# Optimization experiments

Hardware: AMD Instinct MI355X
Metric: run time of the kernel (lower is better)

Reference implementation:

```python
import jax, jax.numpy as jnp
import numpy as np

B, I, H = 128, 512, 512


def setup_inputs() -> dict:
    key = jax.random.key(0)
    ks = jax.random.split(key, 6)
    std = float(1.0 / np.sqrt(H))
    return {
        "x": jax.random.normal(ks[0], (B, I), jnp.float32),
        "h_prev": jax.random.normal(ks[1], (B, H), jnp.float32),
        "C_prev": jax.random.normal(ks[2], (B, H, H), jnp.float32),
        "m_prev": jnp.zeros((B, H), jnp.float32),
        "n_prev": jax.random.normal(ks[3], (B, H), jnp.float32),
        "W": jax.random.uniform(ks[4], (6 * H, I), jnp.float32, -std, std),
        "b": jax.random.uniform(ks[5], (6 * H,), jnp.float32, -std, std),
    }


def reference(x, h_prev, C_prev, m_prev, n_prev, W, b):
    # gates: [B, 6H] -> six [B, H] slices (input, forget, output, query, key, value)
    gates = x @ W.T + b
    ig, fg, og, q, k, v = jnp.split(gates, 6, axis=1)
    inv_sqrt_h = jnp.float32(1.0 / np.sqrt(H))
    k_t = inv_sqrt_h * k
    o_t = jax.nn.sigmoid(og)
    # log-domain stabilizer: log(exp(fg)) == fg, log(exp(ig)) == ig
    m_t = jnp.maximum(fg + m_prev, ig)
    i_t = jnp.exp(ig - m_t)
    f_t = jnp.exp(fg + m_prev - m_t)
    # matrix state update: broadcast-add of (i*v*k) column across last dim (as in source)
    C_t = f_t[:, :, None] * C_prev + (i_t * v * k_t)[:, :, None]  # [B,H,H]
    n_t = f_t * n_prev + i_t * k_t  # [B,H]
    # read-out: C_t @ q and n_t . q
    Cq = jnp.einsum("bij,bj->bi", C_t, q)  # [B,H]
    nq = jnp.einsum("bh,bh->b", n_t, q)  # [B]
    denom = jnp.maximum(jnp.abs(nq), jnp.float32(1e-6))
    h_t = o_t * (Cq / denom[:, None])
    return h_t, C_t, m_t, n_t
```

## Files before the change

### kernel.cpp

```cpp
#include <hip/hip_runtime.h>
#include <math.h>


#define B_SZ   128
#define H_DIM  512
#define I_DIM  512
#define G6     3072
#define BH     65536
#define CSZ    33554432

__global__ __launch_bounds__(256) void gemm_gates(
    const float* __restrict__ x, const float* __restrict__ W,
    const float* __restrict__ bias, float* __restrict__ gates) {
  const int tid = threadIdx.x;
  const int c   = (blockIdx.x % 12) * 256 + tid;
  const int b0  = (blockIdx.x / 12) * 8;

  float acc[8];
#pragma unroll
  for (int j = 0; j < 8; ++j) acc[j] = 0.0f;

  const float4* wrow = reinterpret_cast<const float4*>(W + (size_t)c * I_DIM);
  const float4* x4   = reinterpret_cast<const float4*>(x);

  for (int t4 = 0; t4 < I_DIM / 4; ++t4) {
    float4 wv = wrow[t4];
#pragma unroll
    for (int j = 0; j < 8; ++j) {
      float4 xv = x4[(b0 + j) * (I_DIM / 4) + t4];
      acc[j] += xv.x * wv.x + xv.y * wv.y + xv.z * wv.z + xv.w * wv.w;
    }
  }
  const float bi = bias[c];
#pragma unroll
  for (int j = 0; j < 8; ++j)
    gates[(size_t)(b0 + j) * G6 + c] = acc[j] + bi;
}

__global__ __launch_bounds__(256) void gate_pointwise(
    const float* __restrict__ gates, const float* __restrict__ m_prev,
    const float* __restrict__ n_prev, float* __restrict__ out,
    float* __restrict__ f_arr, float* __restrict__ add_arr,
    float* __restrict__ o_arr, float* __restrict__ invden) {
  const int b   = blockIdx.x;
  const int tid = threadIdx.x;
  const float inv_sqrt_h = 0.044194173824159216f;

  const float* g = gates + (size_t)b * G6;
  float* out_m = out + BH + CSZ;
  float* out_n = out_m + BH;

  float local = 0.0f;
  for (int h = tid; h < H_DIM; h += 256) {
    const float ig = g[h];
    const float fg = g[512 + h];
    const float og = g[1024 + h];
    const float q  = g[1536 + h];
    const float k  = g[2048 + h];
    const float v  = g[2560 + h];

    const int   idx = b * H_DIM + h;
    const float kt  = inv_sqrt_h * k;
    const float ot  = 1.0f / (1.0f + expf(-og));
    const float mp  = m_prev[idx];
    const float npv = n_prev[idx];
    const float mt  = fmaxf(fg + mp, ig);
    const float it  = expf(ig - mt);
    const float ft  = expf(fg + mp - mt);
    const float nt  = ft * npv + it * kt;

    out_m[idx]   = mt;
    out_n[idx]   = nt;
    f_arr[idx]   = ft;
    add_arr[idx] = it * v * kt;
    o_arr[idx]   = ot;
    local += nt * q;
  }

  __shared__ float red[256];
  red[tid] = local;
  __syncthreads();
#pragma unroll
  for (int s = 128; s > 0; s >>= 1) {
    if (tid < s) red[tid] += red[tid + s];
    __syncthreads();
  }
  if (tid == 0) {
    const float denom = fmaxf(fabsf(red[0]), 1e-6f);
    invden[b] = 1.0f / denom;
  }
}

__global__ __launch_bounds__(256) void update_C(
    const float* __restrict__ C_prev, const float* __restrict__ gates,
    const float* __restrict__ f_arr, const float* __restrict__ add_arr,
    const float* __restrict__ o_arr, const float* __restrict__ invden,
    float* __restrict__ out) {
  const int tid  = threadIdx.x;
  const int lane = tid & 63;
  const int r    = blockIdx.x * 4 + (tid >> 6);
  const int b    = r >> 9;

  const float f = f_arr[r];
  const float a = add_arr[r];

  const float4* cp = reinterpret_cast<const float4*>(C_prev) + (size_t)r * 128;
  float4*       ct = reinterpret_cast<float4*>(out + BH) + (size_t)r * 128;
  const float4* q4 = reinterpret_cast<const float4*>(gates + (size_t)b * G6 + 1536);

  float cq = 0.0f;
#pragma unroll
  for (int itr = 0; itr < 2; ++itr) {
    const int idx = lane + 64 * itr;
    const float4 c  = cp[idx];
    const float4 qv = q4[idx];
    float4 o;
    o.x = f * c.x + a;
    o.y = f * c.y + a;
    o.z = f * c.z + a;
    o.w = f * c.w + a;
    ct[idx] = o;
    cq += o.x * qv.x + o.y * qv.y + o.z * qv.z + o.w * qv.w;
  }
#pragma unroll
  for (int off = 32; off > 0; off >>= 1)
    cq += __shfl_xor(cq, off, 64);
  if (lane == 0)
    out[r] = o_arr[r] * cq * invden[b];
}

extern "C" void kernel_launch(void* const* d_in, const int* in_sizes, int n_in,
                              void* d_out, int out_size, void* d_ws, size_t ws_size,
                              hipStream_t stream) {
  const float* x      = (const float*)d_in[0];
  const float* C_prev = (const float*)d_in[2];
  const float* m_prev = (const float*)d_in[3];
  const float* n_prev = (const float*)d_in[4];
  const float* W      = (const float*)d_in[5];
  const float* bias   = (const float*)d_in[6];

  float* out = (float*)d_out;
  float* ws  = (float*)d_ws;

  float* gates   = ws;
  float* f_arr   = ws + 393216;
  float* add_arr = f_arr + BH;
  float* o_arr   = add_arr + BH;
  float* invden  = o_arr + BH;

  gemm_gates<<<192, 256, 0, stream>>>(x, W, bias, gates);
  gate_pointwise<<<B_SZ, 256, 0, stream>>>(gates, m_prev, n_prev, out,
                                           f_arr, add_arr, o_arr, invden);
  update_C<<<BH / 4, 256, 0, stream>>>(C_prev, gates, f_arr, add_arr, o_arr,
                                       invden, out);
}
```

Baseline: 283.8 us.

## Use nontemporal C loads/stores, multi-row blocks, and retune gate GEMM grid

The C-update kernel now has each block process 32 rows (8 per wavefront) with q and invden hoisted out of the loop, and uses nontemporal loads/stores for the 128MB C_prev/C_t streams to avoid cache pollution. The gate GEMM halves the batch rows per block (4 instead of 8) and doubles the grid to increase parallelism. The pointwise kernel uses 512 threads, one per hidden unit. The aim is better streaming bandwidth on the dominant C traffic and higher occupancy for the GEMM, at the cost of more x reloads in the GEMM.

New measurement: 279.4 us. About the same (-1.5%).

```diff
diff --git a/kernel.cpp b/kernel.cpp
--- a/kernel.cpp
+++ b/kernel.cpp
@@ -9,83 +9,82 @@
 #define BH     65536
 #define CSZ    33554432
 
+typedef float f32x4 __attribute__((ext_vector_type(4)));
+
 __global__ __launch_bounds__(256) void gemm_gates(
     const float* __restrict__ x, const float* __restrict__ W,
     const float* __restrict__ bias, float* __restrict__ gates) {
   const int tid = threadIdx.x;
   const int c   = (blockIdx.x % 12) * 256 + tid;
-  const int b0  = (blockIdx.x / 12) * 8;
+  const int b0  = (blockIdx.x / 12) * 4;
 
-  float acc[8];
+  float acc[4];
 #pragma unroll
-  for (int j = 0; j < 8; ++j) acc[j] = 0.0f;
+  for (int j = 0; j < 4; ++j) acc[j] = 0.0f;
 
   const float4* wrow = reinterpret_cast<const float4*>(W + (size_t)c * I_DIM);
   const float4* x4   = reinterpret_cast<const float4*>(x);
 
+#pragma unroll 2
   for (int t4 = 0; t4 < I_DIM / 4; ++t4) {
-    float4 wv = wrow[t4];
+    const float4 wv = wrow[t4];
 #pragma unroll
-    for (int j = 0; j < 8; ++j) {
-      float4 xv = x4[(b0 + j) * (I_DIM / 4) + t4];
+    for (int j = 0; j < 4; ++j) {
+      const float4 xv = x4[(b0 + j) * (I_DIM / 4) + t4];
       acc[j] += xv.x * wv.x + xv.y * wv.y + xv.z * wv.z + xv.w * wv.w;
     }
   }
   const float bi = bias[c];
 #pragma unroll
-  for (int j = 0; j < 8; ++j)
+  for (int j = 0; j < 4; ++j)
     gates[(size_t)(b0 + j) * G6 + c] = acc[j] + bi;
 }
 
-__global__ __launch_bounds__(256) void gate_pointwise(
+__global__ __launch_bounds__(512) void gate_pointwise(
     const float* __restrict__ gates, const float* __restrict__ m_prev,
     const float* __restrict__ n_prev, float* __restrict__ out,
     float* __restrict__ f_arr, float* __restrict__ add_arr,
     float* __restrict__ o_arr, float* __restrict__ invden) {
-  const int b   = blockIdx.x;
-  const int tid = threadIdx.x;
+  const int b = blockIdx.x;
+  const int h = threadIdx.x;
   const float inv_sqrt_h = 0.044194173824159216f;
 
   const float* g = gates + (size_t)b * G6;
   float* out_m = out + BH + CSZ;
   float* out_n = out_m + BH;
 
-  float local = 0.0f;
-  for (int h = tid; h < H_DIM; h += 256) {
-    const float ig = g[h];
-    const float fg = g[512 + h];
-    const float og = g[1024 + h];
-    const float q  = g[1536 + h];
-    const float k  = g[2048 + h];
-    const float v  = g[2560 + h];
+  const float ig = g[h];
+  const float fg = g[512 + h];
+  const float og = g[1024 + h];
+  const float q  = g[1536 + h];
+  const float k  = g[2048 + h];
+  const float v  = g[2560 + h];
 
-    const int   idx = b * H_DIM + h;
-    const float kt  = inv_sqrt_h * k;
-    const float ot  = 1.0f / (1.0f + expf(-og));
-    const float mp  = m_prev[idx];
-    const float npv = n_prev[idx];
-    const float mt  = fmaxf(fg + mp, ig);
-    const float it  = expf(ig - mt);
-    const float ft  = expf(fg + mp - mt);
-    const float nt  = ft * npv + it * kt;
+  const int   idx = b * H_DIM + h;
+  const float kt  = inv_sqrt_h * k;
+  const float ot  = 1.0f / (1.0f + expf(-og));
+  const float mp  = m_prev[idx];
+  const float npv = n_prev[idx];
+  const float mt  = fmaxf(fg + mp, ig);
+  const float it  = expf(ig - mt);
+  const float ft  = expf(fg + mp - mt);
+  const float nt  = ft * npv + it * kt;
 
-    out_m[idx]   = mt;
-    out_n[idx]   = nt;
-    f_arr[idx]   = ft;
-    add_arr[idx] = it * v * kt;
-    o_arr[idx]   = ot;
-    local += nt * q;
-  }
+  out_m[idx]   = mt;
+  out_n[idx]   = nt;
+  f_arr[idx]   = ft;
+  add_arr[idx] = it * v * kt;
+  o_arr[idx]   = ot;
 
-  __shared__ float red[256];
-  red[tid] = local;
+  __shared__ float red[512];
+  red[h] = nt * q;
   __syncthreads();
 #pragma unroll
-  for (int s = 128; s > 0; s >>= 1) {
-    if (tid < s) red[tid] += red[tid + s];
+  for (int s = 256; s > 0; s >>= 1) {
+    if (h < s) red[h] += red[h + s];
     __syncthreads();
   }
-  if (tid == 0) {
+  if (h == 0) {
     const float denom = fmaxf(fabsf(red[0]), 1e-6f);
     invden[b] = 1.0f / denom;
   }
@@ -98,35 +97,44 @@
     float* __restrict__ out) {
   const int tid  = threadIdx.x;
   const int lane = tid & 63;
-  const int r    = blockIdx.x * 4 + (tid >> 6);
-  const int b    = r >> 9;
+  const int w    = tid >> 6;
+  const int r0   = blockIdx.x * 32;
+  const int b    = r0 >> 9;
 
-  const float f = f_arr[r];
-  const float a = add_arr[r];
+  const float4* q4 = reinterpret_cast<const float4*>(gates + (size_t)b * G6 + 1536);
+  const float4 qa = q4[lane];
+  const float4 qb = q4[lane + 64];
+  const float inv_d = invden[b];
 
-  const float4* cp = reinterpret_cast<const float4*>(C_prev) + (size_t)r * 128;
-  float4*       ct = reinterpret_cast<float4*>(out + BH) + (size_t)r * 128;
-  const float4* q4 = reinterpret_cast<const float4*>(gates + (size_t)b * G6 + 1536);
+#pragma unroll 2
+  for (int it = 0; it < 8; ++it) {
+    const int r = r0 + it * 4 + w;
+    const float f = f_arr[r];
+    const float a = add_arr[r];
 
-  float cq = 0.0f;
+    const f32x4* cp = reinterpret_cast<const f32x4*>(C_prev) + (size_t)r * 128;
+    f32x4*       ct = reinterpret_cast<f32x4*>((float*)out + BH) + (size_t)r * 128;
+
+    const f32x4 c0 = __builtin_nontemporal_load(cp + lane);
+    const f32x4 c1 = __builtin_nontemporal_load(cp + lane + 64);
+
+    f32x4 o0, o1;
+    o0.x = f * c0.x + a;  o0.y = f * c0.y + a;
+    o0.z = f * c0.z + a;  o0.w = f * c0.w + a;
+    o1.x = f * c1.x + a;  o1.y = f * c1.y + a;
+    o1.z = f * c1.z + a;  o1.w = f * c1.w + a;
+
+    __builtin_nontemporal_store(o0, ct + lane);
+    __builtin_nontemporal_store(o1, ct + lane + 64);
+
+    float cq = o0.x * qa.x + o0.y * qa.y + o0.z * qa.z + o0.w * qa.w
+             + o1.x * qb.x + o1.y * qb.y + o1.z * qb.z + o1.w * qb.w;
 #pragma unroll
-  for (int itr = 0; itr < 2; ++itr) {
-    const int idx = lane + 64 * itr;
-    const float4 c  = cp[idx];
-    const float4 qv = q4[idx];
-    float4 o;
-    o.x = f * c.x + a;
-    o.y = f * c.y + a;
-    o.z = f * c.z + a;
-    o.w = f * c.w + a;
-    ct[idx] = o;
-    cq += o.x * qv.x + o.y * qv.y + o.z * qv.z + o.w * qv.w;
+    for (int off = 32; off > 0; off >>= 1)
+      cq += __shfl_xor(cq, off, 64);
+    if (lane == 0)
+      out[r] = o_arr[r] * cq * inv_d;
   }
-#pragma unroll
-  for (int off = 32; off > 0; off >>= 1)
-    cq += __shfl_xor(cq, off, 64);
-  if (lane == 0)
-    out[r] = o_arr[r] * cq * invden[b];
 }
 
 extern "C" void kernel_launch(void* const* d_in, const int* in_sizes, int n_in,
@@ -148,9 +156,9 @@
   float* o_arr   = add_arr + BH;
   float* invden  = o_arr + BH;
 
-  gemm_gates<<<192, 256, 0, stream>>>(x, W, bias, gates);
-  gate_pointwise<<<B_SZ, 256, 0, stream>>>(gates, m_prev, n_prev, out,
+  gemm_gates<<<384, 256, 0, stream>>>(x, W, bias, gates);
+  gate_pointwise<<<B_SZ, 512, 0, stream>>>(gates, m_prev, n_prev, out,
                                            f_arr, add_arr, o_arr, invden);
-  update_C<<<BH / 4, 256, 0, stream>>>(C_prev, gates, f_arr, add_arr, o_arr,
-                                       invden, out);
+  update_C<<<BH / 32, 256, 0, stream>>>(C_prev, gates, f_arr, add_arr, o_arr,
+                                        invden, out);
 }
```
